# Optimization experiments

Measured on AMD Instinct MI355X. Metric: run time of the kernel, lower is better.

The kernel has to match this reference:

```python
import jax, jax.numpy as jnp
import numpy as np
from jax import lax

LENGTH, WIDTH = 64, 64
INPUT_DIM = 1


def _convlstm_layer(x_tbchw, W, b):
    """Run one ConvLSTM layer over time. x_tbchw: (L,B,Cin,H,W).
    W: (4*hid, Cin+hid, 3, 3), b: (4*hid,). Returns (outputs (L,B,hid,H,W), last_h)."""
    L, B, _, H, Wd = x_tbchw.shape
    hid = W.shape[0] // 4
    h0 = jnp.zeros((B, hid, H, Wd), dtype=x_tbchw.dtype)
    c0 = jnp.zeros((B, hid, H, Wd), dtype=x_tbchw.dtype)

    def step(carry, xt):
        h, c = carry
        z = lax.conv_general_dilated(
            jnp.concatenate([xt, h], axis=1), W,
            window_strides=(1, 1), padding='SAME',
            dimension_numbers=('NCHW', 'OIHW', 'NCHW'))
        z = z + b[None, :, None, None]
        cc_i, cc_f, cc_o, cc_g = jnp.split(z, 4, axis=1)
        c_next = jax.nn.sigmoid(cc_f) * c + jax.nn.sigmoid(cc_i) * jnp.tanh(cc_g)
        h_next = jax.nn.sigmoid(cc_o) * jnp.tanh(c_next)
        return (h_next, c_next), h_next

    (h_last, _), outs = lax.scan(step, (h0, c0), x_tbchw)
    return outs, h_last


def setup_inputs() -> dict:
    key = jax.random.key(0)
    k1, k2, k3 = jax.random.split(key, 3)
    B, L, N = 16, 12, LENGTH * WIDTH
    emd, out_len = 128, 12
    return {
        'history_data': jax.random.normal(k1, (B, L, N, 1), dtype=jnp.float32),
        'future_data': jnp.zeros((B, L, N, 1), dtype=jnp.float32),
        'W0': jax.random.normal(k2, (4 * emd, INPUT_DIM + emd, 3, 3), dtype=jnp.float32) * 0.05,
        'b0': jnp.zeros((4 * emd,), dtype=jnp.float32),
        'W1': jax.random.normal(k3, (4 * out_len, emd + out_len, 3, 3), dtype=jnp.float32) * 0.05,
        'b1': jnp.zeros((4 * out_len,), dtype=jnp.float32),
        'batch_seen': 0,
        'epoch': 0,
        'train': 1,
    }


def reference(history_data, future_data, W0, b0, W1, b1, batch_seen, epoch, train):
    B, L, N, C = history_data.shape
    # (B,L,1,H,W) -> (L,B,1,H,W) for time-major scan
    x = history_data[..., :INPUT_DIM].reshape(B, L, INPUT_DIM, LENGTH, WIDTH)
    x = jnp.transpose(x, (1, 0, 2, 3, 4))
    outs0, _ = _convlstm_layer(x, W0, b0)          # (L,B,emd,H,W)
    _, h_last = _convlstm_layer(outs0, W1, b1)     # (B,out_len,H,W)
    prediction = h_last.reshape(B, L, LENGTH * WIDTH)[..., None]  # (B,L,N,1)
    return prediction
```

## Files before the change

### kernel.cpp

```cpp
#include <hip/hip_runtime.h>
#include <hip/hip_bf16.h>


typedef __attribute__((ext_vector_type(8))) short short8;
typedef __attribute__((ext_vector_type(4))) float float4v;

#define CS 160
#define KT0 1152
#define KTOT 1440
#define RSTR 2560
#define BSTR 10240
#define BSTR6 15360

__device__ __forceinline__ float sigf(float x) { return 1.f / (1.f + __expf(-x)); }
__device__ __forceinline__ short f2hs(float v) {
  _Float16 h = (_Float16)v;
  return *(short*)&h;
}
__device__ __forceinline__ float bs2f(short s) {
  __hip_bfloat16 h; *(short*)&h = s; return __bfloat162float(h);
}
__device__ __forceinline__ short f2bs(float v) {
  __hip_bfloat16 h = __float2bfloat16(v);
  return *(short*)&h;
}

__device__ __forceinline__ void async_ld16(const short* g, short* l) {
  __builtin_amdgcn_global_load_lds(
      (const __attribute__((address_space(1))) unsigned int*)g,
      (__attribute__((address_space(3))) unsigned int*)l, 16, 0, 0);
}

__device__ __forceinline__ void stage_one(const short* __restrict__ rowPtr, bool rowOK,
                                          short* dstRow, int lane,
                                          const short* __restrict__ zp, int j) {
  int e = j * 64 + lane;
  int px = e >> 2, v = e & 3;
  int xx = px - 1;
  bool ok = rowOK && (px < 66) && (xx >= 0) && (xx < 64);
  const short* g = ok ? (rowPtr + (size_t)xx * CS + v * 8) : zp;
  async_ld16(g, dstRow + e * 8);
}

__device__ __forceinline__ void stage_row(const short* __restrict__ rowPtr, bool rowOK,
                                          short* dstRow, int lane,
                                          const short* __restrict__ zp) {
  #pragma unroll
  for (int j = 0; j < 5; ++j) stage_one(rowPtr, rowOK, dstRow, lane, zp, j);
}

__global__ void detect_dtype(const unsigned short* __restrict__ w0, int* __restrict__ flag) {
  int lane = threadIdx.x;
  int cnt = 0;
  for (int i = 0; i < 4; ++i) {
    unsigned short u = w0[2 * (lane + 64 * i)];
    int e = (u >> 7) & 0xFF;
    unsigned long long b = __ballot(e >= 0xC0);
    cnt += __popcll(b);
  }
  if (lane == 0) *flag = (cnt > 32) ? 1 : 0;
}

__global__ void canon_b(const void* __restrict__ b0, const void* __restrict__ b1,
                        float* __restrict__ Bc0, float* __restrict__ Bc1,
                        const int* __restrict__ flag) {
  int i = blockIdx.x * 256 + threadIdx.x;
  int fl = *flag;
  if (i < 512) {
    float v = fl ? ((const float*)b0)[i] : bs2f(((const short*)b0)[i]);
    if (!isfinite(v) || fabsf(v) > 1e4f) v = 0.f;
    Bc0[i] = v;
  } else if (i < 560) {
    int j = i - 512;
    float v = fl ? ((const float*)b1)[j] : bs2f(((const short*)b1)[j]);
    if (!isfinite(v) || fabsf(v) > 1e4f) v = 0.f;
    Bc1[j] = v;
  }
}

__device__ __forceinline__ float ldw(const void* W, int idx, int fl) {
  float w = fl ? ((const float*)W)[idx] : bs2f(((const short*)W)[idx]);
  if (!isfinite(w) || fabsf(w) > 1e4f) w = 0.f;
  return w;
}

__global__ void prep_w0(const void* __restrict__ W0, short* __restrict__ Wp,
                        const int* __restrict__ flag) {
  int i = blockIdx.x * 256 + threadIdx.x;
  if (i >= 512 * KT0) return;
  int fl = *flag;
  int co = i / KT0, k = i - co * KT0;
  int tap = k >> 7, c = k & 127;
  Wp[i] = f2hs(ldw(W0, (co * 129 + 1 + c) * 9 + tap, fl));
}

__global__ void prep_wx(const void* __restrict__ W0, short* __restrict__ Wx,
                        const int* __restrict__ flag) {
  int i = blockIdx.x * 256 + threadIdx.x;
  if (i >= 512 * 16) return;
  int fl = *flag;
  int co = i >> 4, k = i & 15;
  float w = (k < 9) ? ldw(W0, (co * 129) * 9 + k, fl) : 0.f;
  Wx[i] = f2hs(w);
}

__global__ void prep_w1(const void* __restrict__ W1, short* __restrict__ Wp,
                        const int* __restrict__ flag) {
  int i = blockIdx.x * 256 + threadIdx.x;
  if (i >= 48 * KTOT) return;
  int fl = *flag;
  int co = i / KTOT, k = i - co * KTOT;
  int tap = k / CS, c = k - tap * CS;
  float w = (c < 140) ? ldw(W1, (co * 140 + c) * 9 + tap, fl) : 0.f;
  Wp[i] = f2hs(w);
}

__global__ void prep_xtap(const void* __restrict__ hist, short* __restrict__ Xtap,
                          const int* __restrict__ flag) {
  int i = blockIdx.x * 256 + threadIdx.x;
  int t = i >> 16, p = i & 65535;
  int b = p >> 12, pix = p & 4095, y = pix >> 6, x = pix & 63;
  int fl = *flag;
  short8 lo = {0, 0, 0, 0, 0, 0, 0, 0}, hi = {0, 0, 0, 0, 0, 0, 0, 0};
  #pragma unroll
  for (int k = 0; k < 9; ++k) {
    int dy = k / 3, dx = k - dy * 3;
    int yy = y + dy - 1, xx = x + dx - 1;
    float f = 0.f;
    if (yy >= 0 && yy < 64 && xx >= 0 && xx < 64) {
      int hidx = (b * 12 + t) * 4096 + yy * 64 + xx;
      f = fl ? ((const float*)hist)[hidx] : bs2f(((const short*)hist)[hidx]);
      if (!isfinite(f) || fabsf(f) > 1e4f) f = 0.f;
    }
    if (k < 8) lo[k] = f2hs(f); else hi[k - 8] = f2hs(f);
  }
  *(short8*)(Xtap + (size_t)i * 16) = lo;
  *(short8*)(Xtap + (size_t)i * 16 + 8) = hi;
}

__global__ __launch_bounds__(256, 2) void gemm_gate0(
    const short* __restrict__ Pcur, short* __restrict__ Pnext,
    const short* __restrict__ Wp, const short* __restrict__ Wx,
    const float* __restrict__ Bc0, float* __restrict__ C0,
    const short* __restrict__ Xtap, const short* __restrict__ zp, int t) {
  int pbx = blockIdx.x;
  int xcd = pbx & 7, i = pbx >> 3;
  int mt = xcd * 32 + (i & 31);
  int nt = i >> 5;
  int b = mt >> 4, y0 = (mt & 15) * 4;
  int tid = threadIdx.x, wave = tid >> 6, lane = tid & 63;
  int ln15 = lane & 15, quad = lane >> 4;
  int wm = wave & 1, wn = wave >> 1;
  int hc = nt * 32 + wn * 16 + ln15;

  __shared__ __align__(16) short halo[2 * BSTR6];

  float4v acc[8][4];
  #pragma unroll
  for (int i2 = 0; i2 < 8; ++i2)
    #pragma unroll
    for (int j = 0; j < 4; ++j) acc[i2][j] = (float4v){0.f, 0.f, 0.f, 0.f};

  const short* wbase = Wp + (size_t)hc * KT0 + quad * 8;
  short8 bcur[4], bnxt[4];
  #pragma unroll
  for (int g = 0; g < 4; ++g)
    bcur[g] = *(const short8*)(wbase + (size_t)g * 128 * KT0);

  int yyA = y0 - 1 + wave;
  bool okA = (yyA >= 0) && (yyA < 64);
  const short* baseA = Pcur + (size_t)((b * 64 + yyA) * 64) * CS;
  int yyB = y0 + 3 + wave;
  bool okB = (wave < 2) && (yyB < 64);
  const short* baseB = Pcur + (size_t)((b * 64 + yyB) * 64) * CS;

  bool hiQ = quad >= 2;
  short8 ax[8], bxr[4];
  #pragma unroll
  for (int mf = 0; mf < 8; ++mf) {
    int row = y0 + wm * 2 + (mf >> 2);
    int pixB = (b * 64 + row) * 64 + (mf & 3) * 16 + ln15;
    ax[mf] = *(const short8*)(Xtap + ((size_t)t * 65536 + pixB) * 16 + (quad & 1) * 8);
  }
  #pragma unroll
  for (int g = 0; g < 4; ++g) {
    const short* wxp = Wx + (size_t)(g * 128 + hc) * 16 + (quad & 1) * 8;
    bxr[g] = *(const short8*)(hiQ ? zp : wxp);
  }

  stage_row(baseA, okA, halo + wave * RSTR, lane, zp);
  if (wave < 2) stage_row(baseB, okB, halo + (4 + wave) * RSTR, lane, zp);

  #pragma unroll
  for (int g = 0; g < 4; ++g)
    #pragma unroll
    for (int mf = 0; mf < 8; ++mf)
      acc[mf][g] = __builtin_amdgcn_mfma_f32_16x16x32_f16(ax[mf], bxr[g], acc[mf][g], 0, 0, 0);
  __syncthreads();

  for (int ch = 0; ch < 4; ++ch) {
    int c0 = ch * 32;
    const short* cur = halo + (ch & 1) * BSTR6;
    short* nd = halo + ((ch + 1) & 1) * BSTR6;
    const short* srcA = baseA + c0 + 32;
    const short* srcB = baseB + c0 + 32;
    #pragma unroll
    for (int tap = 0; tap < 9; ++tap) {
      int dy = tap / 3, dx = tap - dy * 3;
      if (ch < 3 && tap < 5) {
        stage_one(srcA, okA, nd + wave * RSTR, lane, zp, tap);
        if (wave < 2) stage_one(srcB, okB, nd + (4 + wave) * RSTR, lane, zp, tap);
      }
      int ntap = (tap < 8) ? tap + 1 : 0;
      int nc0 = (tap < 8) ? c0 : ((ch < 3) ? c0 + 32 : c0);
      #pragma unroll
      for (int g = 0; g < 4; ++g)
        bnxt[g] = *(const short8*)(wbase + (size_t)g * 128 * KT0 + ntap * 128 + nc0);

      short8 af[8];
      #pragma unroll
      for (int mf = 0; mf < 8; ++mf)
        af[mf] = *(const short8*)&cur[(wm * 2 + (mf >> 2) + dy) * RSTR
                                      + ((mf & 3) * 16 + ln15 + dx) * 32 + quad * 8];
      #pragma unroll
      for (int g = 0; g < 4; ++g)
        #pragma unroll
        for (int mf = 0; mf < 8; ++mf)
          acc[mf][g] = __builtin_amdgcn_mfma_f32_16x16x32_f16(af[mf], bcur[g], acc[mf][g], 0, 0, 0);
      #pragma unroll
      for (int g = 0; g < 4; ++g) bcur[g] = bnxt[g];
    }
    __syncthreads();
  }

  float bi = Bc0[hc], bff = Bc0[128 + hc], bo = Bc0[256 + hc], bg = Bc0[384 + hc];
  #pragma unroll
  for (int mf = 0; mf < 8; ++mf) {
    int row = y0 + wm * 2 + (mf >> 2);
    int pixRow = (b * 64 + row) * 64;
    #pragma unroll
    for (int r = 0; r < 4; ++r) {
      int x = (mf & 3) * 16 + quad * 4 + r;
      int pix = pixRow + x;
      float zi = acc[mf][0][r] + bi;
      float zf = acc[mf][1][r] + bff;
      float zo = acc[mf][2][r] + bo;
      float zg = acc[mf][3][r] + bg;
      float cprev = C0[(size_t)pix * 128 + hc];
      float cn = sigf(zf) * cprev + sigf(zi) * tanhf(zg);
      float hn = sigf(zo) * tanhf(cn);
      C0[(size_t)pix * 128 + hc] = cn;
      Pnext[(size_t)pix * CS + hc] = f2hs(hn);
    }
  }
}

__global__ __launch_bounds__(256, 2) void gemm_gate1(
    const short* __restrict__ Prd, short* __restrict__ Pwr,
    const short* __restrict__ Wp, const float* __restrict__ Bc1,
    float* __restrict__ C1, void* __restrict__ outp,
    const short* __restrict__ zp, const int* __restrict__ flagp, int t) {
  int pbx = blockIdx.x;
  int bid = (pbx & 7) * 64 + (pbx >> 3);
  int b = bid >> 5, y0 = (bid & 31) * 2;
  int tid = threadIdx.x, wave = tid >> 6, lane = tid & 63;
  int ln15 = lane & 15, quad = lane >> 4;
  int wr = wave >> 1, wh = wave & 1;
  int flagv = *flagp;

  __shared__ __align__(16) short halo[2 * BSTR];

  float4v acc[2][3];
  #pragma unroll
  for (int i = 0; i < 2; ++i)
    #pragma unroll
    for (int j = 0; j < 3; ++j) acc[i][j] = (float4v){0.f, 0.f, 0.f, 0.f};

  int yy = y0 - 1 + wave;
  bool rowOK = (yy >= 0) && (yy < 64);
  const short* rowBase = Prd + (size_t)((b * 64 + yy) * 64) * CS;

  const short* wbase = Wp + (size_t)ln15 * KTOT + quad * 8;
  short8 bcur[3], bnxt[3];
  #pragma unroll
  for (int nf = 0; nf < 3; ++nf)
    bcur[nf] = *(const short8*)(wbase + (size_t)nf * 16 * KTOT);

  stage_row(rowBase, rowOK, halo + wave * RSTR, lane, zp);
  __syncthreads();

  for (int ch = 0; ch < 5; ++ch) {
    int c0 = ch * 32;
    const short* cur = halo + (ch & 1) * BSTR;
    short* nxtDst = halo + ((ch + 1) & 1) * BSTR + wave * RSTR;
    const short* nxtSrc = rowBase + c0 + 32;
    #pragma unroll
    for (int tap = 0; tap < 9; ++tap) {
      int dy = tap / 3, dx = tap - dy * 3;
      if (ch < 4 && tap < 5)
        stage_one(nxtSrc, rowOK, nxtDst, lane, zp, tap);
      int ntap = (tap < 8) ? tap + 1 : 0;
      int nc0 = (tap < 8) ? c0 : ((ch < 4) ? c0 + 32 : c0);
      #pragma unroll
      for (int nf = 0; nf < 3; ++nf)
        bnxt[nf] = *(const short8*)(wbase + (size_t)nf * 16 * KTOT + ntap * CS + nc0);

      short8 af[2];
      #pragma unroll
      for (int mf = 0; mf < 2; ++mf)
        af[mf] = *(const short8*)&cur[(wr + dy) * RSTR + (wh * 32 + mf * 16 + ln15 + dx) * 32
                                      + quad * 8];
      #pragma unroll
      for (int nf = 0; nf < 3; ++nf)
        #pragma unroll
        for (int mf = 0; mf < 2; ++mf)
          acc[mf][nf] = __builtin_amdgcn_mfma_f32_16x16x32_f16(af[mf], bcur[nf], acc[mf][nf], 0, 0, 0);
      #pragma unroll
      for (int nf = 0; nf < 3; ++nf) bcur[nf] = bnxt[nf];
    }
    __syncthreads();
  }

  float* zbuf = (float*)halo;
  #pragma unroll
  for (int mf = 0; mf < 2; ++mf)
    #pragma unroll
    for (int nf = 0; nf < 3; ++nf)
      #pragma unroll
      for (int r = 0; r < 4; ++r) {
        int pxl = wr * 64 + wh * 32 + mf * 16 + quad * 4 + r;
        zbuf[pxl * 48 + nf * 16 + ln15] = acc[mf][nf][r];
      }
  __syncthreads();

  #pragma unroll
  for (int k = 0; k < 6; ++k) {
    int id = k * 256 + tid;
    int hc = id >> 7, pxl = id & 127;
    float zi = zbuf[pxl * 48 + hc]      + Bc1[hc];
    float zf = zbuf[pxl * 48 + 12 + hc] + Bc1[12 + hc];
    float zo = zbuf[pxl * 48 + 24 + hc] + Bc1[24 + hc];
    float zg = zbuf[pxl * 48 + 36 + hc] + Bc1[36 + hc];
    int y = y0 + (pxl >> 6), x = pxl & 63;
    int pix = (b * 64 + y) * 64 + x;
    float cprev = C1[(size_t)pix * 12 + hc];
    float cn = sigf(zf) * cprev + sigf(zi) * tanhf(zg);
    float hn = sigf(zo) * tanhf(cn);
    C1[(size_t)pix * 12 + hc] = cn;
    Pwr[(size_t)pix * CS + 128 + hc] = f2hs(hn);
    if (t == 11) {
      int oidx = (b * 12 + hc) * 4096 + y * 64 + x;
      if (flagv) ((float*)outp)[oidx] = hn;
      else ((short*)outp)[oidx] = f2bs(hn);
    }
  }
}

extern "C" void kernel_launch(void* const* d_in, const int* in_sizes, int n_in,
                              void* d_out, int out_size, void* d_ws, size_t ws_size,
                              hipStream_t stream) {
  const void* hist = d_in[0];
  const void* W0 = d_in[2];
  const void* b0 = d_in[3];
  const void* W1 = d_in[4];
  const void* b1 = d_in[5];

  char* ws = (char*)d_ws;
  const size_t PszB = (size_t)16 * 4096 * CS * 2;
  short* P[2] = {(short*)ws, (short*)(ws + PszB)};
  float* C0 = (float*)(ws + 2 * PszB);
  const size_t C0e = 2 * PszB + 33554432;
  float* C1 = (float*)(ws + C0e);
  const size_t C1e = C0e + 3145728;
  short* zp = (short*)(ws + C1e);
  const size_t zpe = C1e + 256;
  short* Xtap = (short*)(ws + zpe);
  const size_t Xte = zpe + (size_t)12 * 65536 * 16 * 2;
  short* Wp0 = (short*)(ws + Xte);
  const size_t W0e = Xte + (size_t)512 * KT0 * 2;
  short* Wx0 = (short*)(ws + W0e);
  const size_t Wxe = W0e + 512 * 16 * 2;
  short* Wp1 = (short*)(ws + Wxe);
  const size_t W1e = Wxe + (size_t)48 * KTOT * 2;
  float* Bc0 = (float*)(ws + W1e);
  float* Bc1 = (float*)(ws + W1e + 2048);
  int* flag = (int*)(ws + W1e + 2048 + 192);

  hipMemsetAsync(ws, 0, zpe, stream);
  detect_dtype<<<1, 64, 0, stream>>>((const unsigned short*)W0, flag);
  canon_b<<<3, 256, 0, stream>>>(b0, b1, Bc0, Bc1, flag);
  prep_w0<<<(512 * KT0 + 255) / 256, 256, 0, stream>>>(W0, Wp0, flag);
  prep_wx<<<32, 256, 0, stream>>>(W0, Wx0, flag);
  prep_w1<<<(48 * KTOT + 255) / 256, 256, 0, stream>>>(W1, Wp1, flag);
  prep_xtap<<<3072, 256, 0, stream>>>(hist, Xtap, flag);

  for (int t = 0; t < 12; ++t) {
    gemm_gate0<<<1024, 256, 0, stream>>>(P[t & 1], P[(t + 1) & 1], Wp0, Wx0, Bc0, C0,
                                         Xtap, zp, t);
    gemm_gate1<<<512, 256, 0, stream>>>(P[(t + 1) & 1], P[t & 1], Wp1, Bc1, C1,
                                        d_out, zp, flag, t);
  }
}
```

Baseline: 1.934 ms.

## Shrink LDS halo row stride to raise occupancy of ConvLSTM gate kernels

Each halo row in LDS is cut from 80 to 66 pixel slots (RSTR 2560 to 2112). The async global-to-LDS staging now covers 64 pixels in 4 passes instead of 5. The last pixel and the right zero-pad are filled by a register load that is written back after the MFMA loop. Smaller shared buffers let launch_bounds rise to 3 blocks per CU for gate0 and 4 for gate1, which is meant to hide memory latency. The cost is extra register-held tail data and divergent small writes, plus possible register spills under the tighter occupancy bounds.

```diff
diff --git a/kernel.cpp b/kernel.cpp
--- a/kernel.cpp
+++ b/kernel.cpp
@@ -8,9 +8,9 @@
 #define CS 160
 #define KT0 1152
 #define KTOT 1440
-#define RSTR 2560
-#define BSTR 10240
-#define BSTR6 15360
+#define RSTR 2112
+#define BSTR4 8448
+#define BSTR6 12672
 
 __device__ __forceinline__ float sigf(float x) { return 1.f / (1.f + __expf(-x)); }
 __device__ __forceinline__ short f2hs(float v) {
@@ -31,22 +31,37 @@
       (__attribute__((address_space(3))) unsigned int*)l, 16, 0, 0);
 }
 
-__device__ __forceinline__ void stage_one(const short* __restrict__ rowPtr, bool rowOK,
-                                          short* dstRow, int lane,
-                                          const short* __restrict__ zp, int j) {
+__device__ __forceinline__ void stage_one4(const short* __restrict__ rowPtr, bool rowOK,
+                                           short* dstRow, int lane,
+                                           const short* __restrict__ zp, int j) {
   int e = j * 64 + lane;
   int px = e >> 2, v = e & 3;
   int xx = px - 1;
-  bool ok = rowOK && (px < 66) && (xx >= 0) && (xx < 64);
+  bool ok = rowOK && (xx >= 0);
   const short* g = ok ? (rowPtr + (size_t)xx * CS + v * 8) : zp;
   async_ld16(g, dstRow + e * 8);
 }
 
-__device__ __forceinline__ void stage_row(const short* __restrict__ rowPtr, bool rowOK,
-                                          short* dstRow, int lane,
-                                          const short* __restrict__ zp) {
-  #pragma unroll
-  for (int j = 0; j < 5; ++j) stage_one(rowPtr, rowOK, dstRow, lane, zp, j);
+__device__ __forceinline__ void stage_row4(const short* __restrict__ rowPtr, bool rowOK,
+                                           short* dstRow, int lane,
+                                           const short* __restrict__ zp) {
+  #pragma unroll
+  for (int j = 0; j < 4; ++j) stage_one4(rowPtr, rowOK, dstRow, lane, zp, j);
+}
+
+__device__ __forceinline__ short8 tail_load(const short* __restrict__ srcChunk,
+                                            bool rowOK, int lane) {
+  short8 tv = {0, 0, 0, 0, 0, 0, 0, 0};
+  if (lane < 4 && rowOK) tv = *(const short8*)(srcChunk + (size_t)63 * CS + lane * 8);
+  return tv;
+}
+
+__device__ __forceinline__ void tail_write(short* dstRow, int lane, short8 tv) {
+  if (lane < 8) {
+    short8 w = {0, 0, 0, 0, 0, 0, 0, 0};
+    if (lane < 4) w = tv;
+    *(short8*)(dstRow + (64 + (lane >> 2)) * 32 + (lane & 3) * 8) = w;
+  }
 }
 
 __global__ void detect_dtype(const unsigned short* __restrict__ w0, int* __restrict__ flag) {
@@ -138,7 +153,7 @@
   *(short8*)(Xtap + (size_t)i * 16 + 8) = hi;
 }
 
-__global__ __launch_bounds__(256, 2) void gemm_gate0(
+__global__ __launch_bounds__(256, 3) void gemm_gate0(
     const short* __restrict__ Pcur, short* __restrict__ Pnext,
     const short* __restrict__ Wp, const short* __restrict__ Wx,
     const float* __restrict__ Bc0, float* __restrict__ C0,
@@ -187,15 +202,20 @@
     const short* wxp = Wx + (size_t)(g * 128 + hc) * 16 + (quad & 1) * 8;
     bxr[g] = *(const short8*)(hiQ ? zp : wxp);
   }
-
-  stage_row(baseA, okA, halo + wave * RSTR, lane, zp);
-  if (wave < 2) stage_row(baseB, okB, halo + (4 + wave) * RSTR, lane, zp);
+  short8 tA = tail_load(baseA, okA, lane);
+  short8 tB = tail_load(baseB, okB, lane);
+
+  stage_row4(baseA, okA, halo + wave * RSTR, lane, zp);
+  if (wave < 2) stage_row4(baseB, okB, halo + (4 + wave) * RSTR, lane, zp);
 
   #pragma unroll
   for (int g = 0; g < 4; ++g)
     #pragma unroll
     for (int mf = 0; mf < 8; ++mf)
       acc[mf][g] = __builtin_amdgcn_mfma_f32_16x16x32_f16(ax[mf], bxr[g], acc[mf][g], 0, 0, 0);
+
+  tail_write(halo + wave * RSTR, lane, tA);
+  if (wave < 2) tail_write(halo + (4 + wave) * RSTR, lane, tB);
   __syncthreads();
 
   for (int ch = 0; ch < 4; ++ch) {
@@ -204,12 +224,17 @@
     short* nd = halo + ((ch + 1) & 1) * BSTR6;
     const short* srcA = baseA + c0 + 32;
     const short* srcB = baseB + c0 + 32;
+    short8 nA = {0, 0, 0, 0, 0, 0, 0, 0}, nB = {0, 0, 0, 0, 0, 0, 0, 0};
+    if (ch < 3) {
+      nA = tail_load(srcA, okA, lane);
+      if (wave < 2) nB = tail_load(srcB, okB, lane);
+    }
     #pragma unroll
     for (int tap = 0; tap < 9; ++tap) {
       int dy = tap / 3, dx = tap - dy * 3;
-      if (ch < 3 && tap < 5) {
-        stage_one(srcA, okA, nd + wave * RSTR, lane, zp, tap);
-        if (wave < 2) stage_one(srcB, okB, nd + (4 + wave) * RSTR, lane, zp, tap);
+      if (ch < 3 && tap < 4) {
+        stage_one4(srcA, okA, nd + wave * RSTR, lane, zp, tap);
+        if (wave < 2) stage_one4(srcB, okB, nd + (4 + wave) * RSTR, lane, zp, tap);
       }
       int ntap = (tap < 8) ? tap + 1 : 0;
       int nc0 = (tap < 8) ? c0 : ((ch < 3) ? c0 + 32 : c0);
@@ -229,6 +254,10 @@
           acc[mf][g] = __builtin_amdgcn_mfma_f32_16x16x32_f16(af[mf], bcur[g], acc[mf][g], 0, 0, 0);
       #pragma unroll
       for (int g = 0; g < 4; ++g) bcur[g] = bnxt[g];
+    }
+    if (ch < 3) {
+      tail_write(nd + wave * RSTR, lane, nA);
+      if (wave < 2) tail_write(nd + (4 + wave) * RSTR, lane, nB);
     }
     __syncthreads();
   }
@@ -255,7 +284,7 @@
   }
 }
 
-__global__ __launch_bounds__(256, 2) void gemm_gate1(
+__global__ __launch_bounds__(256, 4) void gemm_gate1(
     const short* __restrict__ Prd, short* __restrict__ Pwr,
     const short* __restrict__ Wp, const float* __restrict__ Bc1,
     float* __restrict__ C1, void* __restrict__ outp,
@@ -268,7 +297,7 @@
   int wr = wave >> 1, wh = wave & 1;
   int flagv = *flagp;
 
-  __shared__ __align__(16) short halo[2 * BSTR];
+  __shared__ __align__(16) short halo[2 * BSTR4];
 
   float4v acc[2][3];
   #pragma unroll
@@ -286,19 +315,23 @@
   for (int nf = 0; nf < 3; ++nf)
     bcur[nf] = *(const short8*)(wbase + (size_t)nf * 16 * KTOT);
 
-  stage_row(rowBase, rowOK, halo + wave * RSTR, lane, zp);
+  short8 tP = tail_load(rowBase, rowOK, lane);
+  stage_row4(rowBase, rowOK, halo + wave * RSTR, lane, zp);
+  tail_write(halo + wave * RSTR, lane, tP);
   __syncthreads();
 
   for (int ch = 0; ch < 5; ++ch) {
     int c0 = ch * 32;
-    const short* cur = halo + (ch & 1) * BSTR;
-    short* nxtDst = halo + ((ch + 1) & 1) * BSTR + wave * RSTR;
+    const short* cur = halo + (ch & 1) * BSTR4;
+    short* nxtDst = halo + ((ch + 1) & 1) * BSTR4 + wave * RSTR;
     const short* nxtSrc = rowBase + c0 + 32;
+    short8 nP = {0, 0, 0, 0, 0, 0, 0, 0};
+    if (ch < 4) nP = tail_load(nxtSrc, rowOK, lane);
     #pragma unroll
     for (int tap = 0; tap < 9; ++tap) {
       int dy = tap / 3, dx = tap - dy * 3;
-      if (ch < 4 && tap < 5)
-        stage_one(nxtSrc, rowOK, nxtDst, lane, zp, tap);
+      if (ch < 4 && tap < 4)
+        stage_one4(nxtSrc, rowOK, nxtDst, lane, zp, tap);
       int ntap = (tap < 8) ? tap + 1 : 0;
       int nc0 = (tap < 8) ? c0 : ((ch < 4) ? c0 + 32 : c0);
       #pragma unroll
@@ -318,6 +351,7 @@
       #pragma unroll
       for (int nf = 0; nf < 3; ++nf) bcur[nf] = bnxt[nf];
     }
+    if (ch < 4) tail_write(nxtDst, lane, nP);
     __syncthreads();
   }
 
```

After: 7.554 ms. 291% more time.
